# Kernel optimization log

Measured on AMD Instinct MI355X. Metric: run time of the kernel, lower is better.

Reference implementation:

```python
import math
import jax, jax.numpy as jnp
import numpy as np

N_INPUTS, N_OUTPUTS = 2049, 1024
OUT_START, OUT_END, IN_END = 25.0, 24000.0, 24000.0


def _build_buffers(n_inputs=N_INPUTS, n_outputs=N_OUTPUTS, output_start=OUT_START,
                   output_end=OUT_END, input_end=IN_END):
    # Mirrors LogScale.__init__ (numpy, construction-time, exact).
    scale = 1.0
    min_log = math.log10(1.0 + scale * output_start)
    max_log = math.log10(1.0 + scale * output_end)
    lin_logs = np.linspace(min_log, max_log, n_outputs, dtype=np.float64)
    freq_per_bin = scale * float(input_end) / (n_inputs - 1)
    center_bins = ((np.power(10.0, lin_logs) - 1.0) / freq_per_bin).astype(np.float32)
    n_linear = 0
    while n_linear < n_outputs - 1 and (center_bins[n_linear + 1] - center_bins[n_linear] <= 1.0 or center_bins[n_linear] < 1.0):
        n_linear += 1
    output_start_idx = center_bins[:n_linear].astype(np.int64)
    fraction_linear = center_bins[:n_linear] - output_start_idx.astype(np.float32)
    linear_pair_idx = (np.concatenate([output_start_idx, output_start_idx + 1])
                       if n_linear > 0 else np.zeros(0, dtype=np.int64))
    n_sum = n_linear
    while n_sum < n_outputs - 2 and (center_bins[n_sum + 1] - center_bins[n_sum] <= 2.0 or center_bins[n_sum] < 2.0):
        n_sum += 1
    fraction_cubic = center_bins[n_linear:n_sum].copy()
    n_tri = n_outputs - n_sum
    ft = center_bins[n_sum:n_sum + n_tri]
    dt = center_bins[n_sum:n_sum + n_tri] - center_bins[n_sum - 1:n_sum - 1 + n_tri]
    weights = np.full((max(n_tri, 1), n_inputs), -np.inf, dtype=np.float32)
    for i in range(n_tri):
        i_mid = int(math.ceil(ft[i]))
        i_start = int(math.ceil(ft[i] - dt[i]))
        i_end = int(math.ceil(ft[i] + dt[i + 1])) if i < n_tri - 1 else i_mid
        weights[i, i_mid] = 0.0
        dist_left = float(i_mid - i_start)
        for ib in range(i_start + 1, i_mid):
            weights[i, ib] = np.float32(10.0 * np.log10(1.0 - (i_mid - ib) / dist_left))
        if i_end > i_mid:
            dist_right = float(i_end - i_mid)
            for ib in range(i_mid + 1, i_end):
                weights[i, ib] = np.float32(10.0 * np.log10(np.float32(1.0 - (ib - i_mid) / dist_right)))
    return linear_pair_idx, fraction_linear, fraction_cubic, weights[:n_tri]


def setup_inputs() -> dict:
    key = jax.random.key(0)
    x = jax.random.normal(key, (32, 512, N_INPUTS), dtype=jnp.float32)
    pidx, flin, fcub, w = _build_buffers()
    return {
        "x": x,
        "fraction_linear": jnp.asarray(flin),
        "fraction_cubic": jnp.asarray(fcub),
        "triangular_weights": jnp.asarray(w),
        "linear_pair_idx": jnp.asarray(pidx, dtype=jnp.int32),
    }


_TRI_CHUNK = 128  # rows of flattened x per lax.map step (bounds the dense intermediate)


def _tri_max(flat, w):
    # (x[:, None, :] + w).max(-1), chunked along N to keep the (chunk, n_tri, n_in)
    # intermediate bounded, mirroring the torch _triangular_amax chunking.
    n, n_in = flat.shape
    pad = (-n) % _TRI_CHUNK
    flat_p = jnp.pad(flat, ((0, pad), (0, 0)))
    xb = flat_p.reshape(-1, _TRI_CHUNK, n_in)
    out = jax.lax.map(lambda xc: jnp.max(xc[:, None, :] + w[None, :, :], axis=-1), xb)
    return out.reshape(-1, w.shape[0])[:n]


def _forward(x, fraction_linear, fraction_cubic, triangular_weights, linear_pair_idx):
    lead = x.shape[:-1]
    n_lin = fraction_linear.shape[0]
    outs = []
    if n_lin > 0:
        pair = jnp.take(x, linear_pair_idx, axis=-1).reshape(*lead, 2, n_lin)
        x0, x1 = pair[..., 0, :], pair[..., 1, :]
        outs.append(x0 + fraction_linear * (x1 - x0))
    if fraction_cubic.shape[0] > 0:
        i0 = jnp.floor(fraction_cubic).astype(jnp.int32)
        f = fraction_cubic - i0.astype(fraction_cubic.dtype)
        g = lambda off: jnp.take(x, i0 + off, axis=-1)
        xm1, xc0, xc1, xc2 = g(-1), g(0), g(1), g(2)
        # Catmull-Rom cubic interpolation at fractional position f in [0,1)
        cubic = xc0 + 0.5 * f * ((xc1 - xm1) + f * ((2.0 * xm1 - 5.0 * xc0 + 4.0 * xc1 - xc2)
                                                    + f * (3.0 * (xc0 - xc1) + xc2 - xm1)))
        outs.append(cubic)
    if triangular_weights.shape[0] > 0:
        flat = x.reshape(-1, x.shape[-1])
        outs.append(_tri_max(flat, triangular_weights).reshape(*lead, triangular_weights.shape[0]))
    return jnp.concatenate(outs, axis=-1)


def reference(x, fraction_linear, fraction_cubic, triangular_weights, linear_pair_idx):
    return _forward(x, fraction_linear, fraction_cubic, triangular_weights, linear_pair_idx)
```

## Files before the change

### kernel.cpp

```cpp
#include <hip/hip_runtime.h>
#include <math.h>

#define NI 2049
#define ROWS 4
#define BT 1024
#define WCAP 4096
#define NTRI_MAX 512

__global__ void logscale_win(const float* __restrict__ w, int n_in,
                             int* __restrict__ tri_start,
                             int* __restrict__ tri_cnt) {
    const int i = blockIdx.x;
    __shared__ int smin, smax;
    if (threadIdx.x == 0) { smin = n_in; smax = -1; }
    __syncthreads();
    int lmin = n_in, lmax = -1;
    const float* wr = w + (size_t)i * n_in;
    for (int b = threadIdx.x; b < n_in; b += blockDim.x) {
        float v = wr[b];
        if (v > -1e30f) { lmin = min(lmin, b); lmax = max(lmax, b); }
    }
    atomicMin(&smin, lmin);
    atomicMax(&smax, lmax);
    __syncthreads();
    if (threadIdx.x == 0) {
        int s = smin, cnt = smax - smin + 1;
        if (cnt < 1) { s = 0; cnt = 1; }
        if (cnt > 64) cnt = 64;
        tri_start[i] = s; tri_cnt[i] = cnt;
    }
}

__global__ void logscale_pack(const float* __restrict__ w,
                              const float* __restrict__ flin,
                              const float* __restrict__ fcub,
                              const int*   __restrict__ pidx,
                              const int*   __restrict__ tri_start,
                              const int*   __restrict__ tri_cnt,
                              float4* __restrict__ meta,
                              float*  __restrict__ wpk,
                              int*    __restrict__ d_total,
                              int n_lin, int n_cub, int n_tri) {
    __shared__ int offs[NTRI_MAX + 1];
    __shared__ int starts[NTRI_MAX];
    const int tid = threadIdx.x;
    for (int i = tid; i < n_tri; i += blockDim.x) {
        offs[i + 1] = tri_cnt[i];
        starts[i]   = tri_start[i];
    }
    if (tid == 0) offs[0] = 0;
    __syncthreads();

    if (tid < 64) {
        int v[8];
        int run = 0;
        const int base = tid * 8;
        #pragma unroll
        for (int k = 0; k < 8; ++k) {
            int idx = base + k;
            int c = (idx < n_tri) ? offs[idx + 1] : 0;
            run += c;
            v[k] = run;
        }
        int tot = run;
        #pragma unroll
        for (int d = 1; d < 64; d <<= 1) {
            int up = __shfl_up(tot, (unsigned)d, 64);
            if (tid >= d) tot += up;
        }
        const int excl = tot - run;
        #pragma unroll
        for (int k = 0; k < 8; ++k) {
            int idx = base + k;
            if (idx < n_tri) offs[idx + 1] = excl + v[k];
        }
    }
    __syncthreads();
    if (tid == 0) {
        int t = offs[n_tri]; if (t > WCAP) t = WCAP;
        *d_total = t;
    }

    const int n_out = n_lin + n_cub + n_tri;
    for (int o = tid; o < n_out; o += blockDim.x) {
        float4 m;
        if (o < n_lin) {
            m.x = __int_as_float(pidx[o]);
            m.y = __int_as_float(pidx[n_lin + o]);
            m.z = flin[o]; m.w = 0.0f;
        } else if (o < n_lin + n_cub) {
            float c = fcub[o - n_lin];
            int i0 = (int)floorf(c);
            m.x = __int_as_float(i0);
            m.y = 0.0f;
            m.z = c - (float)i0; m.w = 0.0f;
        } else {
            int i = o - n_lin - n_cub;
            int oa = min(offs[i], WCAP), ob = min(offs[i + 1], WCAP);
            m.x = __int_as_float(starts[i]);
            m.y = __int_as_float(ob - oa);
            m.z = __int_as_float(oa); m.w = 0.0f;
        }
        meta[o] = m;
    }

    const int wv = tid >> 6, ln = tid & 63;
    for (int i = wv; i < n_tri; i += 4) {
        const int oa = min(offs[i], WCAP);
        const int ob = min(offs[i + 1], WCAP);
        if (ln < ob - oa)
            wpk[oa + ln] = w[(size_t)i * NI + starts[i] + ln];
    }
}

__device__ __forceinline__ void compute_rows4(
    int o, float4 m, const float* __restrict__ xs, const float* __restrict__ wl,
    int n_lin, int n_lc, float res[ROWS]) {
    if (o < n_lin) {
        const int i0 = __float_as_int(m.x);
        const int i1 = __float_as_int(m.y);
        const float f = m.z;
        #pragma unroll
        for (int r = 0; r < ROWS; ++r) {
            const int b = r * NI;
            const float x0 = xs[b + i0];
            const float x1 = xs[b + i1];
            res[r] = x0 + f * (x1 - x0);
        }
    } else if (o < n_lc) {
        const int i0 = __float_as_int(m.x);
        const float f = m.z;
        #pragma unroll
        for (int r = 0; r < ROWS; ++r) {
            const int b = r * NI + i0;
            const float xm1 = xs[b - 1];
            const float x0  = xs[b];
            const float x1  = xs[b + 1];
            const float x2  = xs[b + 2];
            res[r] = x0 + 0.5f * f * (x1 - xm1 +
                     f * (2.0f * xm1 - 5.0f * x0 + 4.0f * x1 - x2 +
                     f * (3.0f * (x0 - x1) + x2 - xm1)));
        }
    } else {
        const int s   = __float_as_int(m.x);
        const int cnt = __float_as_int(m.y);
        const int off = __float_as_int(m.z);
        const float* wj = wl + off;
        const float* xp = xs + s;
        float acc0 = -INFINITY, acc1 = -INFINITY;
        float acc2 = -INFINITY, acc3 = -INFINITY;
        for (int j = 0; j < cnt; ++j) {
            const float wv = wj[j];
            acc0 = fmaxf(acc0, xp[j] + wv);
            acc1 = fmaxf(acc1, xp[j + NI] + wv);
            acc2 = fmaxf(acc2, xp[j + 2 * NI] + wv);
            acc3 = fmaxf(acc3, xp[j + 3 * NI] + wv);
        }
        res[0] = acc0; res[1] = acc1; res[2] = acc2; res[3] = acc3;
    }
}

__global__ __launch_bounds__(BT, 8) void logscale_main(
    const float*  __restrict__ x,
    const float4* __restrict__ meta,
    const float*  __restrict__ wpk,
    const int*    __restrict__ d_total,
    float* __restrict__ out,
    int n_lin, int n_cub, int n_out, int n_rows) {

    __shared__ __align__(16) float xs[ROWS * NI];
    __shared__ __align__(16) float wl[WCAP];

    const int tid  = threadIdx.x;
    const int row0 = blockIdx.x * ROWS;
    const int rows_here = min(ROWS, n_rows - row0);

    float4 m0 = make_float4(0.f, 0.f, 0.f, 0.f);
    if (tid < n_out) m0 = meta[tid];

    const float* xr = x + (size_t)row0 * NI;
    const int nx = rows_here * NI;
    const int nq = nx >> 2;
    const float4* xr4 = (const float4*)xr;
    float4* xs4 = (float4*)xs;
    for (int i = tid; i < nq; i += BT) xs4[i] = xr4[i];
    for (int i = (nq << 2) + tid; i < nx; i += BT) xs[i] = xr[i];

    const int tw  = *d_total;
    const int twq = (tw + 3) >> 2;
    const float4* wp4 = (const float4*)wpk;
    float4* wl4 = (float4*)wl;
    for (int i = tid; i < twq; i += BT) wl4[i] = wp4[i];
    __syncthreads();

    const int n_lc = n_lin + n_cub;
    float* ob = out + (size_t)row0 * n_out;

    if (rows_here == ROWS) {
        float res[ROWS];
        if (tid < n_out) {
            compute_rows4(tid, m0, xs, wl, n_lin, n_lc, res);
            #pragma unroll
            for (int r = 0; r < ROWS; ++r) ob[(size_t)r * n_out + tid] = res[r];
        }
        for (int o = tid + BT; o < n_out; o += BT) {
            const float4 m = meta[o];
            compute_rows4(o, m, xs, wl, n_lin, n_lc, res);
            #pragma unroll
            for (int r = 0; r < ROWS; ++r) ob[(size_t)r * n_out + o] = res[r];
        }
    } else {
        for (int o = tid; o < n_out; o += BT) {
            const float4 m = meta[o];
            for (int r = 0; r < rows_here; ++r) {
                const int b = r * NI;
                float res;
                if (o < n_lin) {
                    const int i0 = __float_as_int(m.x);
                    const int i1 = __float_as_int(m.y);
                    const float f = m.z;
                    const float x0 = xs[b + i0];
                    const float x1 = xs[b + i1];
                    res = x0 + f * (x1 - x0);
                } else if (o < n_lc) {
                    const int i0 = __float_as_int(m.x) + b;
                    const float f = m.z;
                    const float xm1 = xs[i0 - 1];
                    const float x0  = xs[i0];
                    const float x1  = xs[i0 + 1];
                    const float x2  = xs[i0 + 2];
                    res = x0 + 0.5f * f * (x1 - xm1 +
                          f * (2.0f * xm1 - 5.0f * x0 + 4.0f * x1 - x2 +
                          f * (3.0f * (x0 - x1) + x2 - xm1)));
                } else {
                    const int s   = __float_as_int(m.x) + b;
                    const int cnt = __float_as_int(m.y);
                    const int off = __float_as_int(m.z);
                    float mx = -INFINITY;
                    for (int j = 0; j < cnt; ++j)
                        mx = fmaxf(mx, xs[s + j] + wl[off + j]);
                    res = mx;
                }
                ob[(size_t)r * n_out + o] = res;
            }
        }
    }
}

extern "C" void kernel_launch(void* const* d_in, const int* in_sizes, int n_in,
                              void* d_out, int out_size, void* d_ws, size_t ws_size,
                              hipStream_t stream) {
    (void)n_in; (void)ws_size; (void)out_size;
    const float* x    = (const float*)d_in[0];
    const float* flin = (const float*)d_in[1];
    const float* fcub = (const float*)d_in[2];
    const float* w    = (const float*)d_in[3];
    const int*   pidx = (const int*)d_in[4];
    float* out = (float*)d_out;

    const int n_lin  = in_sizes[1];
    const int n_cub  = in_sizes[2];
    const int n_tri  = in_sizes[3] / NI;
    const int n_rows = in_sizes[0] / NI;
    const int n_out  = n_lin + n_cub + n_tri;

    float4* meta      = (float4*)d_ws;
    float*  wpk       = (float*)(meta + n_out);
    int*    tri_start = (int*)(wpk + WCAP);
    int*    tri_cnt   = tri_start + NTRI_MAX;
    int*    d_total   = tri_cnt + NTRI_MAX;

    if (n_tri > 0)
        logscale_win<<<n_tri, 256, 0, stream>>>(w, NI, tri_start, tri_cnt);
    logscale_pack<<<1, 256, 0, stream>>>(w, flin, fcub, pidx, tri_start, tri_cnt,
                                         meta, wpk, d_total, n_lin, n_cub, n_tri);
    const int nblk = (n_rows + ROWS - 1) / ROWS;
    logscale_main<<<nblk, BT, 0, stream>>>(x, meta, wpk, d_total, out,
                                           n_lin, n_cub, n_out, n_rows);
}
```

Measured before the change: 258.8 us.

## Persistent blocks with double-buffered register-prefetched row tiles; read weights from global

Turns the main kernel into a persistent grid of at most 512 blocks that loop over 4-row tiles. The next tile is prefetched into registers while the current tile is computed, then stored into a second shared buffer, so global load latency overlaps compute. The per-block copy of packed triangular weights into shared memory is removed and weights are read directly from global/L1. Partial tiles now read x straight from global. The risk is that double-buffered shared memory (2×32KB) lowers occupancy, and global weight reads may be slower than LDS.

```diff
diff --git a/kernel.cpp b/kernel.cpp
--- a/kernel.cpp
+++ b/kernel.cpp
@@ -6,6 +6,7 @@
 #define BT 1024
 #define WCAP 4096
 #define NTRI_MAX 512
+#define NBLK 512
 
 __global__ void logscale_win(const float* __restrict__ w, int n_in,
                              int* __restrict__ tri_start,
@@ -114,7 +115,7 @@
 }
 
 __device__ __forceinline__ void compute_rows4(
-    int o, float4 m, const float* __restrict__ xs, const float* __restrict__ wl,
+    int o, float4 m, const float* __restrict__ xs, const float* __restrict__ wpk,
     int n_lin, int n_lc, float res[ROWS]) {
     if (o < n_lin) {
         const int i0 = __float_as_int(m.x);
@@ -145,7 +146,7 @@
         const int s   = __float_as_int(m.x);
         const int cnt = __float_as_int(m.y);
         const int off = __float_as_int(m.z);
-        const float* wj = wl + off;
+        const float* wj = wpk + off;
         const float* xp = xs + s;
         float acc0 = -INFINITY, acc1 = -INFINITY;
         float acc2 = -INFINITY, acc3 = -INFINITY;
@@ -160,90 +161,123 @@
     }
 }
 
+__device__ __forceinline__ void tile_load(const float* __restrict__ x, int t,
+                                          int n_rows, int tid,
+                                          float4& v0, float4& v1, float4& v2) {
+    const float4* xr4 = (const float4*)(x + (size_t)t * (ROWS * NI));
+    const int rows_here = min(ROWS, n_rows - t * ROWS);
+    if (rows_here == ROWS) {
+        v0 = xr4[tid];
+        v1 = xr4[tid + BT];
+        if (tid == 0) v2 = xr4[2048];
+    } else {
+        const int nqp = (rows_here * NI) >> 2;
+        if (tid < nqp)      v0 = xr4[tid];
+        if (tid + BT < nqp) v1 = xr4[tid + BT];
+        if (tid == 0 && 2048 < nqp) v2 = xr4[2048];
+    }
+}
+
+__device__ __forceinline__ void tile_store(float* __restrict__ xsbuf, int tid,
+                                           const float4& v0, const float4& v1,
+                                           const float4& v2) {
+    float4* xs4 = (float4*)xsbuf;
+    xs4[tid]      = v0;
+    xs4[tid + BT] = v1;
+    if (tid == 0) xs4[2048] = v2;
+}
+
 __global__ __launch_bounds__(BT, 8) void logscale_main(
     const float*  __restrict__ x,
     const float4* __restrict__ meta,
     const float*  __restrict__ wpk,
-    const int*    __restrict__ d_total,
     float* __restrict__ out,
-    int n_lin, int n_cub, int n_out, int n_rows) {
-
-    __shared__ __align__(16) float xs[ROWS * NI];
-    __shared__ __align__(16) float wl[WCAP];
+    int n_lin, int n_cub, int n_out, int n_rows, int n_tiles) {
+
+    __shared__ __align__(16) float xs[2][ROWS * NI];
 
     const int tid  = threadIdx.x;
-    const int row0 = blockIdx.x * ROWS;
-    const int rows_here = min(ROWS, n_rows - row0);
+    const int n_lc = n_lin + n_cub;
+
+    int t = blockIdx.x;
+    if (t >= n_tiles) return;
 
     float4 m0 = make_float4(0.f, 0.f, 0.f, 0.f);
     if (tid < n_out) m0 = meta[tid];
 
-    const float* xr = x + (size_t)row0 * NI;
-    const int nx = rows_here * NI;
-    const int nq = nx >> 2;
-    const float4* xr4 = (const float4*)xr;
-    float4* xs4 = (float4*)xs;
-    for (int i = tid; i < nq; i += BT) xs4[i] = xr4[i];
-    for (int i = (nq << 2) + tid; i < nx; i += BT) xs[i] = xr[i];
-
-    const int tw  = *d_total;
-    const int twq = (tw + 3) >> 2;
-    const float4* wp4 = (const float4*)wpk;
-    float4* wl4 = (float4*)wl;
-    for (int i = tid; i < twq; i += BT) wl4[i] = wp4[i];
-    __syncthreads();
-
-    const int n_lc = n_lin + n_cub;
-    float* ob = out + (size_t)row0 * n_out;
-
-    if (rows_here == ROWS) {
-        float res[ROWS];
-        if (tid < n_out) {
-            compute_rows4(tid, m0, xs, wl, n_lin, n_lc, res);
-            #pragma unroll
-            for (int r = 0; r < ROWS; ++r) ob[(size_t)r * n_out + tid] = res[r];
-        }
-        for (int o = tid + BT; o < n_out; o += BT) {
-            const float4 m = meta[o];
-            compute_rows4(o, m, xs, wl, n_lin, n_lc, res);
-            #pragma unroll
-            for (int r = 0; r < ROWS; ++r) ob[(size_t)r * n_out + o] = res[r];
-        }
-    } else {
-        for (int o = tid; o < n_out; o += BT) {
-            const float4 m = meta[o];
-            for (int r = 0; r < rows_here; ++r) {
-                const int b = r * NI;
-                float res;
-                if (o < n_lin) {
-                    const int i0 = __float_as_int(m.x);
-                    const int i1 = __float_as_int(m.y);
-                    const float f = m.z;
-                    const float x0 = xs[b + i0];
-                    const float x1 = xs[b + i1];
-                    res = x0 + f * (x1 - x0);
-                } else if (o < n_lc) {
-                    const int i0 = __float_as_int(m.x) + b;
-                    const float f = m.z;
-                    const float xm1 = xs[i0 - 1];
-                    const float x0  = xs[i0];
-                    const float x1  = xs[i0 + 1];
-                    const float x2  = xs[i0 + 2];
-                    res = x0 + 0.5f * f * (x1 - xm1 +
-                          f * (2.0f * xm1 - 5.0f * x0 + 4.0f * x1 - x2 +
-                          f * (3.0f * (x0 - x1) + x2 - xm1)));
-                } else {
-                    const int s   = __float_as_int(m.x) + b;
-                    const int cnt = __float_as_int(m.y);
-                    const int off = __float_as_int(m.z);
-                    float mx = -INFINITY;
-                    for (int j = 0; j < cnt; ++j)
-                        mx = fmaxf(mx, xs[s + j] + wl[off + j]);
-                    res = mx;
+    float4 v0 = make_float4(0.f,0.f,0.f,0.f), v1 = v0, v2 = v0;
+    tile_load(x, t, n_rows, tid, v0, v1, v2);
+    tile_store(xs[0], tid, v0, v1, v2);
+    __syncthreads();
+
+    int cur = 0;
+    while (true) {
+        const int tn = t + gridDim.x;
+        const bool have_next = tn < n_tiles;
+        if (have_next) tile_load(x, tn, n_rows, tid, v0, v1, v2);
+
+        const int row0 = t * ROWS;
+        const int rows_here = min(ROWS, n_rows - row0);
+        float* ob = out + (size_t)row0 * n_out;
+        const float* xsc = xs[cur];
+
+        if (rows_here == ROWS) {
+            float res[ROWS];
+            if (tid < n_out) {
+                compute_rows4(tid, m0, xsc, wpk, n_lin, n_lc, res);
+                #pragma unroll
+                for (int r = 0; r < ROWS; ++r)
+                    ob[(size_t)r * n_out + tid] = res[r];
+            }
+            for (int o = tid + BT; o < n_out; o += BT) {
+                const float4 m = meta[o];
+                compute_rows4(o, m, xsc, wpk, n_lin, n_lc, res);
+                #pragma unroll
+                for (int r = 0; r < ROWS; ++r)
+                    ob[(size_t)r * n_out + o] = res[r];
+            }
+        } else {
+            for (int o = tid; o < n_out; o += BT) {
+                const float4 m = (o == tid) ? m0 : meta[o];
+                for (int r = 0; r < rows_here; ++r) {
+                    const float* xrr = x + (size_t)(row0 + r) * NI;
+                    float res;
+                    if (o < n_lin) {
+                        const int i0 = __float_as_int(m.x);
+                        const int i1 = __float_as_int(m.y);
+                        const float f = m.z;
+                        const float x0 = xrr[i0];
+                        const float x1 = xrr[i1];
+                        res = x0 + f * (x1 - x0);
+                    } else if (o < n_lc) {
+                        const int i0 = __float_as_int(m.x);
+                        const float f = m.z;
+                        const float xm1 = xrr[i0 - 1];
+                        const float x0  = xrr[i0];
+                        const float x1  = xrr[i0 + 1];
+                        const float x2  = xrr[i0 + 2];
+                        res = x0 + 0.5f * f * (x1 - xm1 +
+                              f * (2.0f * xm1 - 5.0f * x0 + 4.0f * x1 - x2 +
+                              f * (3.0f * (x0 - x1) + x2 - xm1)));
+                    } else {
+                        const int s   = __float_as_int(m.x);
+                        const int cnt = __float_as_int(m.y);
+                        const int off = __float_as_int(m.z);
+                        float mx = -INFINITY;
+                        for (int j = 0; j < cnt; ++j)
+                            mx = fmaxf(mx, xrr[s + j] + wpk[off + j]);
+                        res = mx;
+                    }
+                    ob[(size_t)r * n_out + o] = res;
                 }
-                ob[(size_t)r * n_out + o] = res;
             }
         }
+
+        if (!have_next) break;
+        tile_store(xs[cur ^ 1], tid, v0, v1, v2);
+        __syncthreads();
+        cur ^= 1;
+        t = tn;
     }
 }
 
@@ -274,7 +308,8 @@
         logscale_win<<<n_tri, 256, 0, stream>>>(w, NI, tri_start, tri_cnt);
     logscale_pack<<<1, 256, 0, stream>>>(w, flin, fcub, pidx, tri_start, tri_cnt,
                                          meta, wpk, d_total, n_lin, n_cub, n_tri);
-    const int nblk = (n_rows + ROWS - 1) / ROWS;
-    logscale_main<<<nblk, BT, 0, stream>>>(x, meta, wpk, d_total, out,
-                                           n_lin, n_cub, n_out, n_rows);
-}
+    const int n_tiles = (n_rows + ROWS - 1) / ROWS;
+    const int nblk = min(NBLK, n_tiles);
+    logscale_main<<<nblk, BT, 0, stream>>>(x, meta, wpk, out,
+                                           n_lin, n_cub, n_out, n_rows, n_tiles);
+}
```

Result: no change. 261.8 us (+1.1%).
